# Performance work log

Measured on AMD Instinct MI355X. Metric: run time of the kernel, lower is better.

Reference implementation:

```python
import jax, jax.numpy as jnp
import numpy as np

B, S, D, F, T, NS, L, H = 8, 1024, 1024, 4096, 64, 512, 32, 16
TAG_RATE = 0.5      # config.tagging_rate
GSR = 0.5           # config.gate_scaling_rate
ATT_EPS = 1e-12     # config.layer_norm_eps (att_norm)
ENC_EPS = 1e-5      # torch TransformerEncoderLayer default


def _ln(x, g, b, eps):
    m = x.mean(-1, keepdims=True)
    v = x.var(-1, keepdims=True)
    return (x - m) * jax.lax.rsqrt(v + eps) * g + b


def _rope(x):
    # standard rotary embedding over the full hidden dim
    d = x.shape[-1]
    s = x.shape[1]
    inv = 1.0 / (10000.0 ** (jnp.arange(0, d, 2, dtype=jnp.float32) / d))
    ang = jnp.arange(s, dtype=jnp.float32)[:, None] * inv[None, :]  # [S, D/2]
    sin, cos = jnp.sin(ang), jnp.cos(ang)
    x1, x2 = x[..., 0::2], x[..., 1::2]
    return jnp.stack([x1 * cos - x2 * sin, x1 * sin + x2 * cos], axis=-1).reshape(x.shape)


def setup_inputs() -> dict:
    key = jax.random.key(0)
    ks = jax.random.split(key, 24)
    p = lambda k, shp: (0.02 * jax.random.normal(k, shp, dtype=jnp.float32))
    inp = {
        'word_embedding': jax.random.normal(ks[0], (B, S, D), dtype=jnp.float32),
        'attention_mask': jnp.ones((B, S), dtype=jnp.int32),
        'span_batch': jax.random.randint(ks[1], (NS,), 0, B, dtype=jnp.int32),
        'span_start': jax.random.randint(ks[2], (NS,), 0, S - L, dtype=jnp.int32),
        'span_tag': jax.random.randint(ks[3], (NS,), 0, T, dtype=jnp.int32),
        'tag_emb': p(ks[4], (T, D)),
        'gate_w': p(ks[5], (D, 1)),
        'gate_b': jnp.zeros((1,), jnp.float32),
        'attn_ln_g': jnp.ones((D,), jnp.float32),
        'attn_ln_b': jnp.zeros((D,), jnp.float32),
        'in_proj_w': p(ks[6], (3 * D, D)),
        'in_proj_b': jnp.zeros((3 * D,), jnp.float32),
        'out_proj_w': p(ks[7], (D, D)),
        'out_proj_b': jnp.zeros((D,), jnp.float32),
        'enc_ln1_g': jnp.ones((D,), jnp.float32),
        'enc_ln1_b': jnp.zeros((D,), jnp.float32),
        'lin1_w': p(ks[8], (F, D)),
        'lin1_b': jnp.zeros((F,), jnp.float32),
        'lin2_w': p(ks[9], (D, F)),
        'lin2_b': jnp.zeros((D,), jnp.float32),
        'enc_ln2_g': jnp.ones((D,), jnp.float32),
        'enc_ln2_b': jnp.zeros((D,), jnp.float32),
    }
    return inp


def _mha(x, pad, in_proj_w, in_proj_b, out_proj_w, out_proj_b):
    b, s, d = x.shape
    hd = d // H
    qkv = x @ in_proj_w.T + in_proj_b                       # [B,S,3D]
    q, k, v = jnp.split(qkv, 3, axis=-1)
    rs = lambda t: t.reshape(b, s, H, hd).transpose(0, 2, 1, 3)  # [B,H,S,hd]
    q, k, v = rs(q), rs(k), rs(v)
    scores = jnp.einsum('bhqd,bhkd->bhqk', q, k) / jnp.sqrt(jnp.float32(hd))
    scores = jnp.where(pad[:, None, None, :], jnp.float32(-1e30), scores)
    attn = jax.nn.softmax(scores, axis=-1)
    o = jnp.einsum('bhqk,bhkd->bhqd', attn, v).transpose(0, 2, 1, 3).reshape(b, s, d)
    return o @ out_proj_w.T + out_proj_b


def reference(word_embedding, attention_mask, span_batch, span_start, span_tag,
              tag_emb, gate_w, gate_b, attn_ln_g, attn_ln_b,
              in_proj_w, in_proj_b, out_proj_w, out_proj_b,
              enc_ln1_g, enc_ln1_b, lin1_w, lin1_b, lin2_w, lin2_b,
              enc_ln2_g, enc_ln2_b):
    raw = word_embedding                        # dropout off (eval)
    we = _rope(word_embedding)
    # ragged gather -> gate -> scatter-add over fixed-length spans
    tok = span_start[:, None] + jnp.arange(L, dtype=jnp.int32)[None, :]  # [NS,L]
    X = we[span_batch[:, None], tok]            # [NS,L,D]
    gate = GSR * jax.nn.sigmoid(X @ gate_w + gate_b) + (1.0 - GSR) / 2.0  # [NS,L,1]
    res = gate * tag_emb[span_tag][:, None, :] * jnp.float32(L)          # [NS,L,D]
    taged = jnp.zeros_like(word_embedding).at[span_batch[:, None], tok].add(res)
    out_emb = raw + taged * TAG_RATE            # if_merge_by_add
    out_emb = _ln(out_emb, attn_ln_g, attn_ln_b, ATT_EPS)
    pad = attention_mask == 0
    # torch TransformerEncoderLayer (post-norm, relu)
    a = _mha(out_emb, pad, in_proj_w, in_proj_b, out_proj_w, out_proj_b)
    x = _ln(out_emb + a, enc_ln1_g, enc_ln1_b, ENC_EPS)
    ff = jax.nn.relu(x @ lin1_w.T + lin1_b) @ lin2_w.T + lin2_b
    enc = _ln(x + ff, enc_ln2_g, enc_ln2_b, ENC_EPS)
    return enc + out_emb
```

## Files before the change

### kernel.cpp

```cpp
#include <hip/hip_runtime.h>

#define DEV __device__ __forceinline__

typedef short bf16x8 __attribute__((ext_vector_type(8)));
typedef float f32x4 __attribute__((ext_vector_type(4)));
typedef unsigned short u16;
typedef unsigned int u32;

typedef __attribute__((address_space(3))) void lds_void;
typedef __attribute__((address_space(1))) void gbl_void;

DEV void async_copy16(void* lds_dst, const void* g_src) {
    __builtin_amdgcn_global_load_lds((gbl_void*)g_src, (lds_void*)lds_dst, 16, 0, 0);
}

DEV u16 f2bf(float x) {
    u32 u = __float_as_uint(x);
    return (u16)((u + 0x7fffu + ((u >> 16) & 1u)) >> 16);
}
DEV u16 f2bf_fast(float x) {
    return (u16)((__float_as_uint(x) + 0x8000u) >> 16);
}
DEV float bf2f(u16 v) { return __uint_as_float(((u32)v) << 16); }

__global__ __launch_bounds__(256) void f2bf_kernel(const float* __restrict__ src,
                                                   u16* __restrict__ dst, int n4) {
    const int i = blockIdx.x * 256 + threadIdx.x;
    if (i < n4) {
        const float4 v = ((const float4*)src)[i];
        ushort4 o;
        o.x = f2bf(v.x); o.y = f2bf(v.y); o.z = f2bf(v.z); o.w = f2bf(v.w);
        ((ushort4*)dst)[i] = o;
    }
}

__global__ __launch_bounds__(256) void span_kernel(
    const float* __restrict__ we, const int* __restrict__ sb,
    const int* __restrict__ ss, const int* __restrict__ stg,
    const float* __restrict__ tag_emb, const float* __restrict__ gate_w,
    const float* __restrict__ gate_b, float* __restrict__ out_pre) {
    __shared__ float red[4];
    const int n = blockIdx.x >> 5;
    const int l = blockIdx.x & 31;
    const int t = threadIdx.x;
    const int b = sb[n];
    const int s = ss[n] + l;
    const int tag = stg[n];
    const long base = ((long)b * 1024 + s) * 1024;
    float dot = 0.f;
#pragma unroll
    for (int pp = 0; pp < 2; ++pp) {
        const int p = t + pp * 256;
        const float e1 = we[base + 2 * p];
        const float e2 = we[base + 2 * p + 1];
        const float inv = exp2f((float)p * (-13.287712379549449f / 512.0f));
        const float ang = (float)s * inv;
        const float sa = sinf(ang), ca = cosf(ang);
        const float r1 = e1 * ca - e2 * sa;
        const float r2 = e1 * sa + e2 * ca;
        dot += r1 * gate_w[2 * p] + r2 * gate_w[2 * p + 1];
    }
#pragma unroll
    for (int off = 32; off > 0; off >>= 1) dot += __shfl_xor(dot, off, 64);
    if ((t & 63) == 0) red[t >> 6] = dot;
    __syncthreads();
    const float z = red[0] + red[1] + red[2] + red[3] + gate_b[0];
    const float gate = 0.25f + 0.5f / (1.f + __expf(-z));
    const float coef = gate * 16.f;
    const float* te = tag_emb + (long)tag * 1024;
#pragma unroll
    for (int c = 0; c < 4; ++c) {
        const int d = t + c * 256;
        atomicAdd(&out_pre[base + d], coef * te[d]);
    }
}

template <bool WRITE_F32, bool WRITE_BF, bool FINAL>
__global__ __launch_bounds__(256) void ln_kernel(
    const float* __restrict__ X, const float* __restrict__ g,
    const float* __restrict__ bta, float eps, float* __restrict__ Yf,
    u16* __restrict__ Ybf, const u16* __restrict__ addend) {
    __shared__ float red[8];
    const long row = blockIdx.x;
    const int t = threadIdx.x;
    const float4 x = ((const float4*)(X + row * 1024))[t];
    float s = x.x + x.y + x.z + x.w;
#pragma unroll
    for (int off = 32; off > 0; off >>= 1) s += __shfl_xor(s, off, 64);
    if ((t & 63) == 0) red[t >> 6] = s;
    __syncthreads();
    const float mean = (red[0] + red[1] + red[2] + red[3]) * (1.f / 1024.f);
    float4 dx;
    dx.x = x.x - mean; dx.y = x.y - mean; dx.z = x.z - mean; dx.w = x.w - mean;
    float ss = dx.x * dx.x + dx.y * dx.y + dx.z * dx.z + dx.w * dx.w;
#pragma unroll
    for (int off = 32; off > 0; off >>= 1) ss += __shfl_xor(ss, off, 64);
    if ((t & 63) == 0) red[4 + (t >> 6)] = ss;
    __syncthreads();
    const float var = (red[4] + red[5] + red[6] + red[7]) * (1.f / 1024.f);
    const float rstd = rsqrtf(var + eps);
    const float4 gv = ((const float4*)g)[t];
    const float4 bv = ((const float4*)bta)[t];
    float4 y;
    y.x = dx.x * rstd * gv.x + bv.x;
    y.y = dx.y * rstd * gv.y + bv.y;
    y.z = dx.z * rstd * gv.z + bv.z;
    y.w = dx.w * rstd * gv.w + bv.w;
    if (FINAL) {
        const ushort4 a = ((const ushort4*)(addend + row * 1024))[t];
        y.x += bf2f(a.x); y.y += bf2f(a.y); y.z += bf2f(a.z); y.w += bf2f(a.w);
    }
    if (WRITE_F32) ((float4*)(Yf + row * 1024))[t] = y;
    if (WRITE_BF) {
        ushort4 o;
        o.x = f2bf(y.x); o.y = f2bf(y.y); o.z = f2bf(y.z); o.w = f2bf(y.w);
        ((ushort4*)(Ybf + row * 1024))[t] = o;
    }
}

template <bool OUT_BF16, bool RELU, bool HAS_RES>
__global__ __launch_bounds__(256, 2) void gemm_nt(
    const u16* __restrict__ A, const u16* __restrict__ B,
    const float* __restrict__ bias, const u16* __restrict__ res,
    void* __restrict__ Cout, int N, int K) {
    __shared__ u16 Al[8192];
    __shared__ u16 Bl[8192];
    const int tid = threadIdx.x;
    const int wave = tid >> 6;
    const int lane = tid & 63;
    const int quad = lane >> 4;
    const int lq = lane & 15;
    const int wm = wave >> 1;
    const int wn = wave & 1;
    const long rowBase = (long)blockIdx.x * 128;
    const long colBase = (long)blockIdx.y * 128;

    f32x4 acc[4][4];
    const f32x4 fzero = {0.f, 0.f, 0.f, 0.f};
#pragma unroll
    for (int i = 0; i < 4; ++i)
#pragma unroll
        for (int j = 0; j < 4; ++j) acc[i][j] = fzero;

    const int rX = tid >> 3;
    const int pX = (tid & 7) ^ (rX & 7);
    const u16* gA = A + (rowBase + rX) * (long)K + pX * 8;
    const u16* gB = B + (colBase + rX) * (long)K + pX * 8;
    u16* ldsA = Al + wave * 512;
    u16* ldsB = Bl + wave * 512;

    for (int kt = 0; kt < K; kt += 64) {
        __syncthreads();
#pragma unroll
        for (int c = 0; c < 4; ++c) {
            async_copy16(ldsA + c * 2048, gA + (long)c * 32 * K + kt);
            async_copy16(ldsB + c * 2048, gB + (long)c * 32 * K + kt);
        }
        __syncthreads();
#pragma unroll
        for (int ks = 0; ks < 2; ++ks) {
            bf16x8 af[4], bfr[4];
#pragma unroll
            for (int i = 0; i < 4; ++i) {
                const int r = wm * 64 + i * 16 + lq;
                af[i] = *(const bf16x8*)&Al[r * 64 + (((ks * 4 + quad) ^ (lq & 7)) * 8)];
            }
#pragma unroll
            for (int j = 0; j < 4; ++j) {
                const int r = wn * 64 + j * 16 + lq;
                bfr[j] = *(const bf16x8*)&Bl[r * 64 + (((ks * 4 + quad) ^ (lq & 7)) * 8)];
            }
#pragma unroll
            for (int i = 0; i < 4; ++i)
#pragma unroll
                for (int j = 0; j < 4; ++j)
                    acc[i][j] = __builtin_amdgcn_mfma_f32_16x16x32_bf16(
                        af[i], bfr[j], acc[i][j], 0, 0, 0);
        }
    }

    float biasv[4];
#pragma unroll
    for (int j = 0; j < 4; ++j) biasv[j] = bias[colBase + wn * 64 + j * 16 + lq];
#pragma unroll
    for (int i = 0; i < 4; ++i) {
        const long grow = rowBase + wm * 64 + i * 16 + quad * 4;
#pragma unroll
        for (int j = 0; j < 4; ++j) {
            const long gcol = colBase + wn * 64 + j * 16 + lq;
#pragma unroll
            for (int r = 0; r < 4; ++r) {
                float v = acc[i][j][r] + biasv[j];
                if (RELU) v = fmaxf(v, 0.f);
                if (HAS_RES) v += bf2f(res[(grow + r) * N + gcol]);
                if (OUT_BF16)
                    ((u16*)Cout)[(grow + r) * N + gcol] = f2bf(v);
                else
                    ((float*)Cout)[(grow + r) * N + gcol] = v;
            }
        }
    }
}

#define PH_SYNC()                                          \
    do {                                                   \
        __builtin_amdgcn_s_barrier();                      \
        asm volatile("s_waitcnt lgkmcnt(0)" ::: "memory"); \
        __builtin_amdgcn_sched_barrier(0);                 \
    } while (0)

template <bool RELU>
__global__ __launch_bounds__(512, 2) void gemm_nt8(
    const u16* __restrict__ A, const u16* __restrict__ B,
    const float* __restrict__ bias, u16* __restrict__ Cout, int N, int K) {
    __shared__ u16 Al[2][16384];
    __shared__ u16 Bl[2][16384];
    const int tid = threadIdx.x;
    const int wave = tid >> 6;
    const int lane = tid & 63;
    const int quad = lane >> 4;
    const int lq = lane & 15;
    const int lq7 = lq & 7;
    const int wm = wave >> 2;
    const int wn = wave & 3;
    const long rowBase = (long)blockIdx.x * 256;
    const long colBase = (long)blockIdx.y * 256;
    const int NT = K >> 6;

    const int rs = tid >> 3;
    const int js = (tid & 7) ^ (rs & 7);
    const u16* gA = A + (rowBase + rs) * (long)K + js * 8;
    const u16* gB = B + (colBase + rs) * (long)K + js * 8;

    f32x4 acc[8][4];
    const f32x4 fz = {0.f, 0.f, 0.f, 0.f};
#pragma unroll
    for (int i = 0; i < 8; ++i)
#pragma unroll
        for (int j = 0; j < 4; ++j) acc[i][j] = fz;

    auto stA = [&](int buf, int h, int t) {
        u16* d = &Al[buf][h * 8192 + wave * 512];
        const u16* s = gA + (long)h * 128 * K + t * 64;
        async_copy16(d, s);
        async_copy16(d + 4096, s + (long)64 * K);
    };
    auto stB = [&](int buf, int h, int t) {
        u16* d = &Bl[buf][h * 8192 + wave * 512];
        const u16* s = gB + (long)h * 128 * K + t * 64;
        async_copy16(d, s);
        async_copy16(d + 4096, s + (long)64 * K);
    };
    auto ldA = [&](int buf, int i, int kh) {
        const int r = wm * 128 + i * 16 + lq;
        return *(const bf16x8*)&Al[buf][r * 64 + ((((kh << 2) | quad) ^ lq7) << 3)];
    };
    auto ldB = [&](int buf, int j, int kh) {
        const int r = wn * 64 + j * 16 + lq;
        return *(const bf16x8*)&Bl[buf][r * 64 + ((((kh << 2) | quad) ^ lq7) << 3)];
    };

    stA(0, 0, 0); stA(0, 1, 0); stB(0, 0, 0); stB(0, 1, 0);
    stA(1, 0, 1);
    asm volatile("s_waitcnt vmcnt(2)" ::: "memory");
    __builtin_amdgcn_s_barrier();

    bf16x8 at[8], ab[8], bl[4], br[4];
    for (int it = 0; it < (NT >> 1); ++it) {
        const int t1 = 2 * it + 1;
        int t2 = 2 * it + 2; if (t2 >= NT) t2 -= NT;
        int t3 = 2 * it + 3; if (t3 >= NT) t3 -= NT;

#pragma unroll
        for (int i = 0; i < 4; ++i) { at[2 * i] = ldA(0, i, 0); at[2 * i + 1] = ldA(0, i, 1); }
#pragma unroll
        for (int j = 0; j < 2; ++j) { bl[2 * j] = ldB(0, j, 0); bl[2 * j + 1] = ldB(0, j, 1); }
        stA(1, 1, t1);
        PH_SYNC();
        __builtin_amdgcn_s_setprio(1);
#pragma unroll
        for (int i = 0; i < 4; ++i)
#pragma unroll
            for (int j = 0; j < 2; ++j)
#pragma unroll
                for (int kh = 0; kh < 2; ++kh)
                    acc[i][j] = __builtin_amdgcn_mfma_f32_16x16x32_bf16(
                        at[2 * i + kh], bl[2 * j + kh], acc[i][j], 0, 0, 0);
        __builtin_amdgcn_s_setprio(0);
        __builtin_amdgcn_s_barrier();
#pragma unroll
        for (int j = 0; j < 2; ++j) { br[2 * j] = ldB(0, j + 2, 0); br[2 * j + 1] = ldB(0, j + 2, 1); }
        stB(1, 0, t1);
        PH_SYNC();
        __builtin_amdgcn_s_setprio(1);
#pragma unroll
        for (int i = 0; i < 4; ++i)
#pragma unroll
            for (int j = 0; j < 2; ++j)
#pragma unroll
                for (int kh = 0; kh < 2; ++kh)
                    acc[i][j + 2] = __builtin_amdgcn_mfma_f32_16x16x32_bf16(
                        at[2 * i + kh], br[2 * j + kh], acc[i][j + 2], 0, 0, 0);
        __builtin_amdgcn_s_setprio(0);
        __builtin_amdgcn_s_barrier();
#pragma unroll
        for (int i = 0; i < 4; ++i) { ab[2 * i] = ldA(0, i + 4, 0); ab[2 * i + 1] = ldA(0, i + 4, 1); }
        stB(1, 1, t1);
        PH_SYNC();
        __builtin_amdgcn_s_setprio(1);
#pragma unroll
        for (int i = 0; i < 4; ++i)
#pragma unroll
            for (int j = 0; j < 2; ++j)
#pragma unroll
                for (int kh = 0; kh < 2; ++kh)
                    acc[i + 4][j] = __builtin_amdgcn_mfma_f32_16x16x32_bf16(
                        ab[2 * i + kh], bl[2 * j + kh], acc[i + 4][j], 0, 0, 0);
        __builtin_amdgcn_s_setprio(0);
        __builtin_amdgcn_s_barrier();
        stA(0, 0, t2);
        PH_SYNC();
        __builtin_amdgcn_s_setprio(1);
#pragma unroll
        for (int i = 0; i < 4; ++i)
#pragma unroll
            for (int j = 0; j < 2; ++j)
#pragma unroll
                for (int kh = 0; kh < 2; ++kh)
                    acc[i + 4][j + 2] = __builtin_amdgcn_mfma_f32_16x16x32_bf16(
                        ab[2 * i + kh], br[2 * j + kh], acc[i + 4][j + 2], 0, 0, 0);
        __builtin_amdgcn_s_setprio(0);
        asm volatile("s_waitcnt vmcnt(2)" ::: "memory");
        __builtin_amdgcn_s_barrier();

#pragma unroll
        for (int i = 0; i < 4; ++i) { at[2 * i] = ldA(1, i, 0); at[2 * i + 1] = ldA(1, i, 1); }
#pragma unroll
        for (int j = 0; j < 2; ++j) { bl[2 * j] = ldB(1, j, 0); bl[2 * j + 1] = ldB(1, j, 1); }
        stA(0, 1, t2);
        PH_SYNC();
        __builtin_amdgcn_s_setprio(1);
#pragma unroll
        for (int i = 0; i < 4; ++i)
#pragma unroll
            for (int j = 0; j < 2; ++j)
#pragma unroll
                for (int kh = 0; kh < 2; ++kh)
                    acc[i][j] = __builtin_amdgcn_mfma_f32_16x16x32_bf16(
                        at[2 * i + kh], bl[2 * j + kh], acc[i][j], 0, 0, 0);
        __builtin_amdgcn_s_setprio(0);
        __builtin_amdgcn_s_barrier();
#pragma unroll
        for (int j = 0; j < 2; ++j) { br[2 * j] = ldB(1, j + 2, 0); br[2 * j + 1] = ldB(1, j + 2, 1); }
        stB(0, 0, t2);
        PH_SYNC();
        __builtin_amdgcn_s_setprio(1);
#pragma unroll
        for (int i = 0; i < 4; ++i)
#pragma unroll
            for (int j = 0; j < 2; ++j)
#pragma unroll
                for (int kh = 0; kh < 2; ++kh)
                    acc[i][j + 2] = __builtin_amdgcn_mfma_f32_16x16x32_bf16(
                        at[2 * i + kh], br[2 * j + kh], acc[i][j + 2], 0, 0, 0);
        __builtin_amdgcn_s_setprio(0);
        __builtin_amdgcn_s_barrier();
#pragma unroll
        for (int i = 0; i < 4; ++i) { ab[2 * i] = ldA(1, i + 4, 0); ab[2 * i + 1] = ldA(1, i + 4, 1); }
        stB(0, 1, t2);
        PH_SYNC();
        __builtin_amdgcn_s_setprio(1);
#pragma unroll
        for (int i = 0; i < 4; ++i)
#pragma unroll
            for (int j = 0; j < 2; ++j)
#pragma unroll
                for (int kh = 0; kh < 2; ++kh)
                    acc[i + 4][j] = __builtin_amdgcn_mfma_f32_16x16x32_bf16(
                        ab[2 * i + kh], bl[2 * j + kh], acc[i + 4][j], 0, 0, 0);
        __builtin_amdgcn_s_setprio(0);
        __builtin_amdgcn_s_barrier();
        stA(1, 0, t3);
        PH_SYNC();
        __builtin_amdgcn_s_setprio(1);
#pragma unroll
        for (int i = 0; i < 4; ++i)
#pragma unroll
            for (int j = 0; j < 2; ++j)
#pragma unroll
                for (int kh = 0; kh < 2; ++kh)
                    acc[i + 4][j + 2] = __builtin_amdgcn_mfma_f32_16x16x32_bf16(
                        ab[2 * i + kh], br[2 * j + kh], acc[i + 4][j + 2], 0, 0, 0);
        __builtin_amdgcn_s_setprio(0);
        asm volatile("s_waitcnt vmcnt(2)" ::: "memory");
        __builtin_amdgcn_s_barrier();
    }

    asm volatile("s_waitcnt vmcnt(0)" ::: "memory");
    float bv[4];
#pragma unroll
    for (int j = 0; j < 4; ++j) bv[j] = bias[colBase + wn * 64 + j * 16 + lq];
#pragma unroll
    for (int i = 0; i < 8; ++i) {
        const long grow = rowBase + wm * 128 + i * 16 + quad * 4;
#pragma unroll
        for (int j = 0; j < 4; ++j) {
            const long gcol = colBase + wn * 64 + j * 16 + lq;
#pragma unroll
            for (int r = 0; r < 4; ++r) {
                float v = acc[i][j][r] + bv[j];
                if (RELU) v = fmaxf(v, 0.f);
                Cout[(grow + r) * N + gcol] = f2bf(v);
            }
        }
    }
}

__global__ __launch_bounds__(256) void vtrans_kernel(const u16* __restrict__ QKV,
                                                     u16* __restrict__ Vt) {
    __shared__ u16 tile[64][72];
    const int bid = blockIdx.x;
    const int st = bid & 15;
    const int h = (bid >> 4) & 15;
    const int b = bid >> 8;
    const int t = threadIdx.x;
    const int sl = t >> 2;
    const int dc = (t & 3) * 16;
    const u16* src = QKV + ((long)(b * 1024 + st * 64 + sl)) * 3072 + 2048 + h * 64 + dc;
    *(uint4*)&tile[sl][dc] = *(const uint4*)src;
    *(uint4*)&tile[sl][dc + 8] = *(const uint4*)(src + 8);
    __syncthreads();
    const int dl = t >> 2;
    const int sc = (t & 3) * 16;
    union { u16 u[16]; uint4 q[2]; } tmp;
#pragma unroll
    for (int i = 0; i < 16; ++i) tmp.u[i] = tile[sc + i][dl];
    u16* dst = Vt + ((long)(b * 16 + h) * 64 + dl) * 1024 + st * 64 + sc;
    *(uint4*)dst = tmp.q[0];
    *(uint4*)(dst + 8) = tmp.q[1];
}

__global__ __launch_bounds__(256, 4) void attn_kernel(
    const u16* __restrict__ QKV, const u16* __restrict__ Vt,
    const int* __restrict__ mask, u16* __restrict__ Out) {
    __shared__ u16 KL[4096];
    __shared__ u16 VL[4096];
    __shared__ u16 PL[4][16 * 72];
    const int tid = threadIdx.x;
    const int wid = tid >> 6;
    const int lane = tid & 63;
    const int quad = lane >> 4;
    const int lq = lane & 15;
    const int slot0 = quad ^ (lq & 7);
    const int slot1 = slot0 ^ 4;

    const int bid = blockIdx.x;
    const int qb = bid & 7;
    const int h = (bid >> 3) & 15;
    const int b = bid >> 7;
    const int qbase = qb * 128 + wid * 32;

    bf16x8 aq[2][2];
#pragma unroll
    for (int t = 0; t < 2; ++t) {
        const u16* qp = QKV + ((long)(b * 1024 + qbase + t * 16 + lq)) * 3072 +
                        h * 64 + quad * 8;
        aq[t][0] = *(const bf16x8*)qp;
        aq[t][1] = *(const bf16x8*)(qp + 32);
    }

    const int c0 = tid, c1 = 256 + tid;
    const int r0 = c0 >> 3, j0 = (c0 & 7) ^ (r0 & 7);
    const int r1 = c1 >> 3, j1 = (c1 & 7) ^ (r1 & 7);
    const u16* srcK0 = QKV + ((long)(b * 1024 + r0)) * 3072 + 1024 + h * 64 + j0 * 8;
    const u16* srcK1 = QKV + ((long)(b * 1024 + r1)) * 3072 + 1024 + h * 64 + j1 * 8;
    const u16* srcV0 = Vt + ((long)(b * 16 + h) * 64 + r0) * 1024 + j0 * 8;
    const u16* srcV1 = Vt + ((long)(b * 16 + h) * 64 + r1) * 1024 + j1 * 8;
    u16* ldsK0 = KL + wid * 512;
    u16* ldsK1 = KL + 2048 + wid * 512;
    u16* ldsV0 = VL + wid * 512;
    u16* ldsV1 = VL + 2048 + wid * 512;

    const f32x4 fzero = {0.f, 0.f, 0.f, 0.f};
    f32x4 acc[2][4];
#pragma unroll
    for (int t = 0; t < 2; ++t)
#pragma unroll
        for (int j = 0; j < 4; ++j) acc[t][j] = fzero;
    float lsum[2][4] = {{0.f, 0.f, 0.f, 0.f}, {0.f, 0.f, 0.f, 0.f}};
    u16* myP = PL[wid];
    const int* mrow = mask + b * 1024;

    for (int kt = 0; kt < 1024; kt += 64) {
        __syncthreads();
        async_copy16(ldsK0, srcK0 + (long)kt * 3072);
        async_copy16(ldsK1, srcK1 + (long)kt * 3072);
        async_copy16(ldsV0, srcV0 + kt);
        async_copy16(ldsV1, srcV1 + kt);
        __syncthreads();

        bf16x8 kf0[4], kf1[4];
#pragma unroll
        for (int ct = 0; ct < 4; ++ct) {
            const int rowb = (ct * 16 + lq) * 64;
            kf0[ct] = *(const bf16x8*)&KL[rowb + slot0 * 8];
            kf1[ct] = *(const bf16x8*)&KL[rowb + slot1 * 8];
        }
        float mw[4];
#pragma unroll
        for (int ct = 0; ct < 4; ++ct) mw[ct] = mrow[kt + ct * 16 + lq] ? 1.f : 0.f;

#pragma unroll
        for (int t = 0; t < 2; ++t) {
            f32x4 s[4];
#pragma unroll
            for (int ct = 0; ct < 4; ++ct) {
                s[ct] = __builtin_amdgcn_mfma_f32_16x16x32_bf16(aq[t][0], kf0[ct],
                                                                fzero, 0, 0, 0);
                s[ct] = __builtin_amdgcn_mfma_f32_16x16x32_bf16(aq[t][1], kf1[ct],
                                                                s[ct], 0, 0, 0);
            }
            asm volatile("s_waitcnt lgkmcnt(0)" ::: "memory");
#pragma unroll
            for (int ct = 0; ct < 4; ++ct)
#pragma unroll
                for (int r = 0; r < 4; ++r) {
                    const float p = mw[ct] * __expf(s[ct][r] * 0.125f);
                    lsum[t][r] += p;
                    myP[(quad * 4 + r) * 72 + ct * 16 + lq] = f2bf_fast(p);
                }
            asm volatile("s_waitcnt lgkmcnt(0)" ::: "memory");
            const bf16x8 pf0 = *(const bf16x8*)&myP[lq * 72 + quad * 8];
            const bf16x8 pf1 = *(const bf16x8*)&myP[lq * 72 + 32 + quad * 8];
#pragma unroll
            for (int j = 0; j < 4; ++j) {
                const int rowb = (j * 16 + lq) * 64;
                const bf16x8 vf0 = *(const bf16x8*)&VL[rowb + slot0 * 8];
                const bf16x8 vf1 = *(const bf16x8*)&VL[rowb + slot1 * 8];
                acc[t][j] = __builtin_amdgcn_mfma_f32_16x16x32_bf16(pf0, vf0,
                                                                    acc[t][j], 0, 0, 0);
                acc[t][j] = __builtin_amdgcn_mfma_f32_16x16x32_bf16(pf1, vf1,
                                                                    acc[t][j], 0, 0, 0);
            }
        }
    }

#pragma unroll
    for (int t = 0; t < 2; ++t) {
        float inv[4];
#pragma unroll
        for (int r = 0; r < 4; ++r) {
            float l = lsum[t][r];
#pragma unroll
            for (int off = 1; off < 16; off <<= 1) l += __shfl_xor(l, off, 16);
            inv[r] = 1.f / l;
        }
        const long orow = (long)b * 1024 + qbase + t * 16 + quad * 4;
#pragma unroll
        for (int j = 0; j < 4; ++j)
#pragma unroll
            for (int r = 0; r < 4; ++r)
                Out[(orow + r) * 1024 + h * 64 + j * 16 + lq] =
                    f2bf_fast(acc[t][j][r] * inv[r]);
    }
}

extern "C" void kernel_launch(void* const* d_in, const int* in_sizes, int n_in,
                              void* d_out, int out_size, void* d_ws, size_t ws_size,
                              hipStream_t stream) {
    const float* we        = (const float*)d_in[0];
    const int*   amask     = (const int*)d_in[1];
    const int*   span_b    = (const int*)d_in[2];
    const int*   span_s    = (const int*)d_in[3];
    const int*   span_t    = (const int*)d_in[4];
    const float* tag_emb   = (const float*)d_in[5];
    const float* gate_w    = (const float*)d_in[6];
    const float* gate_b    = (const float*)d_in[7];
    const float* attn_ln_g = (const float*)d_in[8];
    const float* attn_ln_b = (const float*)d_in[9];
    const float* in_proj_w = (const float*)d_in[10];
    const float* in_proj_b = (const float*)d_in[11];
    const float* out_proj_w= (const float*)d_in[12];
    const float* out_proj_b= (const float*)d_in[13];
    const float* enc1_g    = (const float*)d_in[14];
    const float* enc1_b    = (const float*)d_in[15];
    const float* lin1_w    = (const float*)d_in[16];
    const float* lin1_b    = (const float*)d_in[17];
    const float* lin2_w    = (const float*)d_in[18];
    const float* lin2_b    = (const float*)d_in[19];
    const float* enc2_g    = (const float*)d_in[20];
    const float* enc2_b    = (const float*)d_in[21];
    float* out = (float*)d_out;

    char* ws = (char*)d_ws;
    size_t off = 0;
    auto alloc = [&](size_t bytes) {
        void* p = ws + off;
        off += (bytes + 255) & ~(size_t)255;
        return p;
    };
    const size_t MT = 8192;
    u16* oe_bf   = (u16*)alloc(MT * 1024 * 2);
    u16* ax_bf   = (u16*)alloc(MT * 1024 * 2);
    char* region = (char*)alloc((size_t)67108864);
    u16* qkv_bf  = (u16*)region;
    u16* vt_bf   = (u16*)(region + (size_t)MT * 3072 * 2);
    u16* ff1_bf  = (u16*)region;
    u16* wb_inproj  = (u16*)alloc((size_t)3072 * 1024 * 2);
    u16* wb_outproj = (u16*)alloc((size_t)1024 * 1024 * 2);
    u16* wb_lin1    = (u16*)alloc((size_t)4096 * 1024 * 2);
    u16* wb_lin2    = (u16*)alloc((size_t)1024 * 4096 * 2);

    hipMemcpyAsync(out, we, MT * 1024 * 4, hipMemcpyDeviceToDevice, stream);
    f2bf_kernel<<<3072, 256, 0, stream>>>(in_proj_w, wb_inproj, 3072 * 1024 / 4);
    f2bf_kernel<<<1024, 256, 0, stream>>>(out_proj_w, wb_outproj, 1024 * 1024 / 4);
    f2bf_kernel<<<4096, 256, 0, stream>>>(lin1_w, wb_lin1, 4096 * 1024 / 4);
    f2bf_kernel<<<4096, 256, 0, stream>>>(lin2_w, wb_lin2, 1024 * 4096 / 4);
    span_kernel<<<16384, 256, 0, stream>>>(we, span_b, span_s, span_t, tag_emb,
                                           gate_w, gate_b, out);
    ln_kernel<false, true, false><<<8192, 256, 0, stream>>>(
        out, attn_ln_g, attn_ln_b, 1e-12f, nullptr, oe_bf, nullptr);
    dim3 g1(32, 12);
    gemm_nt8<false><<<g1, 512, 0, stream>>>(oe_bf, wb_inproj, in_proj_b,
                                            qkv_bf, 3072, 1024);
    vtrans_kernel<<<2048, 256, 0, stream>>>(qkv_bf, vt_bf);
    attn_kernel<<<1024, 256, 0, stream>>>(qkv_bf, vt_bf, amask, ax_bf);
    dim3 g2(64, 8);
    gemm_nt<false, false, true><<<g2, 256, 0, stream>>>(ax_bf, wb_outproj, out_proj_b,
                                                        oe_bf, out, 1024, 1024);
    ln_kernel<false, true, false><<<8192, 256, 0, stream>>>(
        out, enc1_g, enc1_b, 1e-5f, nullptr, ax_bf, nullptr);
    dim3 g3(32, 16);
    gemm_nt8<true><<<g3, 512, 0, stream>>>(ax_bf, wb_lin1, lin1_b,
                                           ff1_bf, 4096, 1024);
    gemm_nt<false, false, true><<<g2, 256, 0, stream>>>(ff1_bf, wb_lin2, lin2_b,
                                                        ax_bf, out, 1024, 4096);
    ln_kernel<true, false, true><<<8192, 256, 0, stream>>>(
        out, enc2_g, enc2_b, 1e-5f, out, nullptr, oe_bf);
}
```

Before: 570.1 us.

## Fuse span tagging, LN and weight casts; fold V transpose into QKV GEMM

Replaces the memcpy, four weight-cast kernels, the atomic span scatter and the first layernorm with a single prep kernel. In it each token row finds its overlapping spans via ballots and adds the tag embeddings in registers before normalising. The QKV GEMM epilogue writes V directly in transposed layout, which removes the separate vtrans kernel. The 8-wave GEMM's async-load schedule is reordered so B for the next tile is prefetched first. Attention block indexing is permuted to group heads and batches per query block. These changes cut launches, atomics and global traffic, at the cost of strided scattered stores for V and a per-row scan over all 512 spans.

```diff
diff --git a/kernel.cpp b/kernel.cpp
--- a/kernel.cpp
+++ b/kernel.cpp
@@ -6,6 +6,7 @@
 typedef float f32x4 __attribute__((ext_vector_type(4)));
 typedef unsigned short u16;
 typedef unsigned int u32;
+typedef unsigned long long u64;
 
 typedef __attribute__((address_space(3))) void lds_void;
 typedef __attribute__((address_space(1))) void gbl_void;
@@ -23,42 +24,62 @@
 }
 DEV float bf2f(u16 v) { return __uint_as_float(((u32)v) << 16); }
 
-__global__ __launch_bounds__(256) void f2bf_kernel(const float* __restrict__ src,
-                                                   u16* __restrict__ dst, int n4) {
-    const int i = blockIdx.x * 256 + threadIdx.x;
-    if (i < n4) {
+__global__ __launch_bounds__(256) void prep_kernel(
+    const float* __restrict__ we, const int* __restrict__ sb,
+    const int* __restrict__ ss, const int* __restrict__ stg,
+    const float* __restrict__ tag_emb, const float* __restrict__ gate_w,
+    const float* __restrict__ gate_b, const float* __restrict__ g,
+    const float* __restrict__ bta,
+    const float* __restrict__ w0, const float* __restrict__ w1,
+    const float* __restrict__ w2, const float* __restrict__ w3,
+    u16* __restrict__ oe_bf, u16* __restrict__ o0, u16* __restrict__ o1,
+    u16* __restrict__ o2, u16* __restrict__ o3) {
+    const int blk = blockIdx.x;
+    const int t = threadIdx.x;
+
+    if (blk >= 8192) {
+        int base = blk - 8192;
+        const float* src; u16* dst;
+        if (base < 3072)      { src = w0; dst = o0; }
+        else if (base < 4096) { src = w1; dst = o1; base -= 3072; }
+        else if (base < 8192) { src = w2; dst = o2; base -= 4096; }
+        else                  { src = w3; dst = o3; base -= 8192; }
+        const int i = base * 256 + t;
         const float4 v = ((const float4*)src)[i];
         ushort4 o;
         o.x = f2bf(v.x); o.y = f2bf(v.y); o.z = f2bf(v.z); o.w = f2bf(v.w);
         ((ushort4*)dst)[i] = o;
-    }
-}
-
-__global__ __launch_bounds__(256) void span_kernel(
-    const float* __restrict__ we, const int* __restrict__ sb,
-    const int* __restrict__ ss, const int* __restrict__ stg,
-    const float* __restrict__ tag_emb, const float* __restrict__ gate_w,
-    const float* __restrict__ gate_b, float* __restrict__ out_pre) {
-    __shared__ float red[4];
-    const int n = blockIdx.x >> 5;
-    const int l = blockIdx.x & 31;
-    const int t = threadIdx.x;
-    const int b = sb[n];
-    const int s = ss[n] + l;
-    const int tag = stg[n];
-    const long base = ((long)b * 1024 + s) * 1024;
-    float dot = 0.f;
-#pragma unroll
-    for (int pp = 0; pp < 2; ++pp) {
-        const int p = t + pp * 256;
-        const float e1 = we[base + 2 * p];
-        const float e2 = we[base + 2 * p + 1];
-        const float inv = exp2f((float)p * (-13.287712379549449f / 512.0f));
-        const float ang = (float)s * inv;
-        const float sa = sinf(ang), ca = cosf(ang);
-        const float r1 = e1 * ca - e2 * sa;
-        const float r2 = e1 * sa + e2 * ca;
-        dot += r1 * gate_w[2 * p] + r2 * gate_w[2 * p + 1];
+        return;
+    }
+
+    __shared__ float red[8];
+    __shared__ u64 smask[8];
+    const int row = blk;
+    const int b = row >> 10;
+    const int s = row & 1023;
+
+    {
+        const bool m0 = (sb[t] == b) && ((u32)(s - ss[t]) < 32u);
+        const bool m1 = (sb[t + 256] == b) && ((u32)(s - ss[t + 256]) < 32u);
+        const u64 b0 = __ballot(m0);
+        const u64 b1 = __ballot(m1);
+        if ((t & 63) == 0) { smask[t >> 6] = b0; smask[4 + (t >> 6)] = b1; }
+    }
+
+    float4 x = ((const float4*)(we + (long)row * 1024))[t];
+    const float4 gw = ((const float4*)gate_w)[t];
+    float dot;
+    {
+        const float p0 = (float)(2 * t);
+        const float p1 = (float)(2 * t + 1);
+        const float inv0 = exp2f(p0 * (-13.287712379549449f / 512.0f));
+        const float inv1 = exp2f(p1 * (-13.287712379549449f / 512.0f));
+        const float a0 = (float)s * inv0, a1 = (float)s * inv1;
+        const float s0 = sinf(a0), c0 = cosf(a0);
+        const float s1 = sinf(a1), c1 = cosf(a1);
+        const float r1a = x.x * c0 - x.y * s0, r2a = x.x * s0 + x.y * c0;
+        const float r1b = x.z * c1 - x.w * s1, r2b = x.z * s1 + x.w * c1;
+        dot = r1a * gw.x + r2a * gw.y + r1b * gw.z + r2b * gw.w;
     }
 #pragma unroll
     for (int off = 32; off > 0; off >>= 1) dot += __shfl_xor(dot, off, 64);
@@ -67,12 +88,47 @@
     const float z = red[0] + red[1] + red[2] + red[3] + gate_b[0];
     const float gate = 0.25f + 0.5f / (1.f + __expf(-z));
     const float coef = gate * 16.f;
-    const float* te = tag_emb + (long)tag * 1024;
-#pragma unroll
-    for (int c = 0; c < 4; ++c) {
-        const int d = t + c * 256;
-        atomicAdd(&out_pre[base + d], coef * te[d]);
-    }
+
+    float4 add = {0.f, 0.f, 0.f, 0.f};
+#pragma unroll
+    for (int gi = 0; gi < 8; ++gi) {
+        u64 m = smask[gi];
+        const int nb = (gi & 3) * 64 + (gi >> 2) * 256;
+        while (m) {
+            const int bit = __ffsll(m) - 1;
+            m &= m - 1;
+            const int tag = stg[nb + bit];
+            const float4 te = ((const float4*)(tag_emb + (long)tag * 1024))[t];
+            add.x += te.x; add.y += te.y; add.z += te.z; add.w += te.w;
+        }
+    }
+    x.x += coef * add.x; x.y += coef * add.y;
+    x.z += coef * add.z; x.w += coef * add.w;
+
+    __syncthreads();
+    float sm = x.x + x.y + x.z + x.w;
+#pragma unroll
+    for (int off = 32; off > 0; off >>= 1) sm += __shfl_xor(sm, off, 64);
+    if ((t & 63) == 0) red[t >> 6] = sm;
+    __syncthreads();
+    const float mean = (red[0] + red[1] + red[2] + red[3]) * (1.f / 1024.f);
+    float4 dx;
+    dx.x = x.x - mean; dx.y = x.y - mean; dx.z = x.z - mean; dx.w = x.w - mean;
+    float ss2 = dx.x * dx.x + dx.y * dx.y + dx.z * dx.z + dx.w * dx.w;
+#pragma unroll
+    for (int off = 32; off > 0; off >>= 1) ss2 += __shfl_xor(ss2, off, 64);
+    if ((t & 63) == 0) red[4 + (t >> 6)] = ss2;
+    __syncthreads();
+    const float var = (red[4] + red[5] + red[6] + red[7]) * (1.f / 1024.f);
+    const float rstd = rsqrtf(var + 1e-12f);
+    const float4 gv = ((const float4*)g)[t];
+    const float4 bv = ((const float4*)bta)[t];
+    ushort4 o;
+    o.x = f2bf(dx.x * rstd * gv.x + bv.x);
+    o.y = f2bf(dx.y * rstd * gv.y + bv.y);
+    o.z = f2bf(dx.z * rstd * gv.z + bv.z);
+    o.w = f2bf(dx.w * rstd * gv.w + bv.w);
+    ((ushort4*)(oe_bf + (long)row * 1024))[t] = o;
 }
 
 template <bool WRITE_F32, bool WRITE_BF, bool FINAL>
@@ -118,11 +174,11 @@
     }
 }
 
-template <bool OUT_BF16, bool RELU, bool HAS_RES>
+template <bool OUT_BF16, bool RELU, bool HAS_RES, bool VTRANS>
 __global__ __launch_bounds__(256, 2) void gemm_nt(
     const u16* __restrict__ A, const u16* __restrict__ B,
     const float* __restrict__ bias, const u16* __restrict__ res,
-    void* __restrict__ Cout, int N, int K) {
+    void* __restrict__ Cout, int N, int K, u16* __restrict__ vt) {
     __shared__ u16 Al[8192];
     __shared__ u16 Bl[8192];
     const int tid = threadIdx.x;
@@ -193,26 +249,28 @@
                 float v = acc[i][j][r] + biasv[j];
                 if (RELU) v = fmaxf(v, 0.f);
                 if (HAS_RES) v += bf2f(res[(grow + r) * N + gcol]);
-                if (OUT_BF16)
+                if (VTRANS && gcol >= 2048) {
+                    const int hh = (int)(gcol - 2048) >> 6;
+                    const int dd = (int)(gcol - 2048) & 63;
+                    const long rr = grow + r;
+                    const int bb = (int)(rr >> 10);
+                    const int sR = (int)(rr & 1023);
+                    vt[(((long)bb * 16 + hh) * 64 + dd) * 1024 + sR] = f2bf(v);
+                } else if (OUT_BF16) {
                     ((u16*)Cout)[(grow + r) * N + gcol] = f2bf(v);
-                else
+                } else {
                     ((float*)Cout)[(grow + r) * N + gcol] = v;
+                }
             }
         }
     }
 }
 
-#define PH_SYNC()                                          \
-    do {                                                   \
-        __builtin_amdgcn_s_barrier();                      \
-        asm volatile("s_waitcnt lgkmcnt(0)" ::: "memory"); \
-        __builtin_amdgcn_sched_barrier(0);                 \
-    } while (0)
-
-template <bool RELU>
+template <bool RELU, bool VTRANS>
 __global__ __launch_bounds__(512, 2) void gemm_nt8(
     const u16* __restrict__ A, const u16* __restrict__ B,
-    const float* __restrict__ bias, u16* __restrict__ Cout, int N, int K) {
+    const float* __restrict__ bias, u16* __restrict__ Cout, int N, int K,
+    u16* __restrict__ vt) {
     __shared__ u16 Al[2][16384];
     __shared__ u16 Bl[2][16384];
     const int tid = threadIdx.x;
@@ -241,13 +299,13 @@
 
     auto stA = [&](int buf, int h, int t) {
         u16* d = &Al[buf][h * 8192 + wave * 512];
-        const u16* s = gA + (long)h * 128 * K + t * 64;
+        const u16* s = gA + (long)h * 128 * K + (long)t * 64;
         async_copy16(d, s);
         async_copy16(d + 4096, s + (long)64 * K);
     };
     auto stB = [&](int buf, int h, int t) {
         u16* d = &Bl[buf][h * 8192 + wave * 512];
-        const u16* s = gB + (long)h * 128 * K + t * 64;
+        const u16* s = gB + (long)h * 128 * K + (long)t * 64;
         async_copy16(d, s);
         async_copy16(d + 4096, s + (long)64 * K);
     };
@@ -260,9 +318,16 @@
         return *(const bf16x8*)&Bl[buf][r * 64 + ((((kh << 2) | quad) ^ lq7) << 3)];
     };
 
+#define PH_SYNC()                               \
+    do {                                        \
+        __builtin_amdgcn_s_barrier();           \
+        asm volatile("s_waitcnt lgkmcnt(0)");   \
+    } while (0)
+
     stA(0, 0, 0); stA(0, 1, 0); stB(0, 0, 0); stB(0, 1, 0);
-    stA(1, 0, 1);
-    asm volatile("s_waitcnt vmcnt(2)" ::: "memory");
+    stB(1, 0, 1); stB(1, 1, 1);
+    asm volatile("s_waitcnt vmcnt(4)");
+    __builtin_amdgcn_sched_barrier(0);
     __builtin_amdgcn_s_barrier();
 
     bf16x8 at[8], ab[8], bl[4], br[4];
@@ -275,7 +340,7 @@
         for (int i = 0; i < 4; ++i) { at[2 * i] = ldA(0, i, 0); at[2 * i + 1] = ldA(0, i, 1); }
 #pragma unroll
         for (int j = 0; j < 2; ++j) { bl[2 * j] = ldB(0, j, 0); bl[2 * j + 1] = ldB(0, j, 1); }
-        stA(1, 1, t1);
+        stA(1, 0, t1);
         PH_SYNC();
         __builtin_amdgcn_s_setprio(1);
 #pragma unroll
@@ -290,7 +355,7 @@
         __builtin_amdgcn_s_barrier();
 #pragma unroll
         for (int j = 0; j < 2; ++j) { br[2 * j] = ldB(0, j + 2, 0); br[2 * j + 1] = ldB(0, j + 2, 1); }
-        stB(1, 0, t1);
+        stA(1, 1, t1);
         PH_SYNC();
         __builtin_amdgcn_s_setprio(1);
 #pragma unroll
@@ -305,7 +370,7 @@
         __builtin_amdgcn_s_barrier();
 #pragma unroll
         for (int i = 0; i < 4; ++i) { ab[2 * i] = ldA(0, i + 4, 0); ab[2 * i + 1] = ldA(0, i + 4, 1); }
-        stB(1, 1, t1);
+        stB(0, 0, t2);
         PH_SYNC();
         __builtin_amdgcn_s_setprio(1);
 #pragma unroll
@@ -318,7 +383,7 @@
                         ab[2 * i + kh], bl[2 * j + kh], acc[i + 4][j], 0, 0, 0);
         __builtin_amdgcn_s_setprio(0);
         __builtin_amdgcn_s_barrier();
-        stA(0, 0, t2);
+        stB(0, 1, t2);
         PH_SYNC();
         __builtin_amdgcn_s_setprio(1);
 #pragma unroll
@@ -330,14 +395,15 @@
                     acc[i + 4][j + 2] = __builtin_amdgcn_mfma_f32_16x16x32_bf16(
                         ab[2 * i + kh], br[2 * j + kh], acc[i + 4][j + 2], 0, 0, 0);
         __builtin_amdgcn_s_setprio(0);
-        asm volatile("s_waitcnt vmcnt(2)" ::: "memory");
+        asm volatile("s_waitcnt vmcnt(4)");
+        __builtin_amdgcn_sched_barrier(0);
         __builtin_amdgcn_s_barrier();
 
 #pragma unroll
         for (int i = 0; i < 4; ++i) { at[2 * i] = ldA(1, i, 0); at[2 * i + 1] = ldA(1, i, 1); }
 #pragma unroll
         for (int j = 0; j < 2; ++j) { bl[2 * j] = ldB(1, j, 0); bl[2 * j + 1] = ldB(1, j, 1); }
-        stA(0, 1, t2);
+        stA(0, 0, t2);
         PH_SYNC();
         __builtin_amdgcn_s_setprio(1);
 #pragma unroll
@@ -352,7 +418,7 @@
         __builtin_amdgcn_s_barrier();
 #pragma unroll
         for (int j = 0; j < 2; ++j) { br[2 * j] = ldB(1, j + 2, 0); br[2 * j + 1] = ldB(1, j + 2, 1); }
-        stB(0, 0, t2);
+        stA(0, 1, t2);
         PH_SYNC();
         __builtin_amdgcn_s_setprio(1);
 #pragma unroll
@@ -367,7 +433,7 @@
         __builtin_amdgcn_s_barrier();
 #pragma unroll
         for (int i = 0; i < 4; ++i) { ab[2 * i] = ldA(1, i + 4, 0); ab[2 * i + 1] = ldA(1, i + 4, 1); }
-        stB(0, 1, t2);
+        stB(1, 0, t3);
         PH_SYNC();
         __builtin_amdgcn_s_setprio(1);
 #pragma unroll
@@ -380,7 +446,7 @@
                         ab[2 * i + kh], bl[2 * j + kh], acc[i + 4][j], 0, 0, 0);
         __builtin_amdgcn_s_setprio(0);
         __builtin_amdgcn_s_barrier();
-        stA(1, 0, t3);
+        stB(1, 1, t3);
         PH_SYNC();
         __builtin_amdgcn_s_setprio(1);
 #pragma unroll
@@ -392,11 +458,13 @@
                     acc[i + 4][j + 2] = __builtin_amdgcn_mfma_f32_16x16x32_bf16(
                         ab[2 * i + kh], br[2 * j + kh], acc[i + 4][j + 2], 0, 0, 0);
         __builtin_amdgcn_s_setprio(0);
-        asm volatile("s_waitcnt vmcnt(2)" ::: "memory");
-        __builtin_amdgcn_s_barrier();
-    }
-
-    asm volatile("s_waitcnt vmcnt(0)" ::: "memory");
+        asm volatile("s_waitcnt vmcnt(4)");
+        __builtin_amdgcn_sched_barrier(0);
+        __builtin_amdgcn_s_barrier();
+    }
+#undef PH_SYNC
+
+    asm volatile("s_waitcnt vmcnt(0)");
     float bv[4];
 #pragma unroll
     for (int j = 0; j < 4; ++j) bv[j] = bias[colBase + wn * 64 + j * 16 + lq];
@@ -410,34 +478,19 @@
             for (int r = 0; r < 4; ++r) {
                 float v = acc[i][j][r] + bv[j];
                 if (RELU) v = fmaxf(v, 0.f);
-                Cout[(grow + r) * N + gcol] = f2bf(v);
+                if (VTRANS && gcol >= 2048) {
+                    const int hh = (int)(gcol - 2048) >> 6;
+                    const int dd = (int)(gcol - 2048) & 63;
+                    const long rr = grow + r;
+                    const int bb = (int)(rr >> 10);
+                    const int sR = (int)(rr & 1023);
+                    vt[(((long)bb * 16 + hh) * 64 + dd) * 1024 + sR] = f2bf(v);
+                } else {
+                    Cout[(grow + r) * N + gcol] = f2bf(v);
+                }
             }
         }
     }
-}
-
-__global__ __launch_bounds__(256) void vtrans_kernel(const u16* __restrict__ QKV,
-                                                     u16* __restrict__ Vt) {
-    __shared__ u16 tile[64][72];
-    const int bid = blockIdx.x;
-    const int st = bid & 15;
-    const int h = (bid >> 4) & 15;
-    const int b = bid >> 8;
-    const int t = threadIdx.x;
-    const int sl = t >> 2;
-    const int dc = (t & 3) * 16;
-    const u16* src = QKV + ((long)(b * 1024 + st * 64 + sl)) * 3072 + 2048 + h * 64 + dc;
-    *(uint4*)&tile[sl][dc] = *(const uint4*)src;
-    *(uint4*)&tile[sl][dc + 8] = *(const uint4*)(src + 8);
-    __syncthreads();
-    const int dl = t >> 2;
-    const int sc = (t & 3) * 16;
-    union { u16 u[16]; uint4 q[2]; } tmp;
-#pragma unroll
-    for (int i = 0; i < 16; ++i) tmp.u[i] = tile[sc + i][dl];
-    u16* dst = Vt + ((long)(b * 16 + h) * 64 + dl) * 1024 + st * 64 + sc;
-    *(uint4*)dst = tmp.q[0];
-    *(uint4*)(dst + 8) = tmp.q[1];
 }
 
 __global__ __launch_bounds__(256, 4) void attn_kernel(
@@ -455,9 +508,9 @@
     const int slot1 = slot0 ^ 4;
 
     const int bid = blockIdx.x;
-    const int qb = bid & 7;
-    const int h = (bid >> 3) & 15;
-    const int b = bid >> 7;
+    const int qb = bid >> 7;
+    const int h = bid & 15;
+    const int b = (bid >> 4) & 7;
     const int qbase = qb * 128 + wid * 32;
 
     bf16x8 aq[2][2];
@@ -611,30 +664,24 @@
     u16* wb_lin1    = (u16*)alloc((size_t)4096 * 1024 * 2);
     u16* wb_lin2    = (u16*)alloc((size_t)1024 * 4096 * 2);
 
-    hipMemcpyAsync(out, we, MT * 1024 * 4, hipMemcpyDeviceToDevice, stream);
-    f2bf_kernel<<<3072, 256, 0, stream>>>(in_proj_w, wb_inproj, 3072 * 1024 / 4);
-    f2bf_kernel<<<1024, 256, 0, stream>>>(out_proj_w, wb_outproj, 1024 * 1024 / 4);
-    f2bf_kernel<<<4096, 256, 0, stream>>>(lin1_w, wb_lin1, 4096 * 1024 / 4);
-    f2bf_kernel<<<4096, 256, 0, stream>>>(lin2_w, wb_lin2, 1024 * 4096 / 4);
-    span_kernel<<<16384, 256, 0, stream>>>(we, span_b, span_s, span_t, tag_emb,
-                                           gate_w, gate_b, out);
-    ln_kernel<false, true, false><<<8192, 256, 0, stream>>>(
-        out, attn_ln_g, attn_ln_b, 1e-12f, nullptr, oe_bf, nullptr);
+    prep_kernel<<<20480, 256, 0, stream>>>(
+        we, span_b, span_s, span_t, tag_emb, gate_w, gate_b,
+        attn_ln_g, attn_ln_b, in_proj_w, out_proj_w, lin1_w, lin2_w,
+        oe_bf, wb_inproj, wb_outproj, wb_lin1, wb_lin2);
     dim3 g1(32, 12);
-    gemm_nt8<false><<<g1, 512, 0, stream>>>(oe_bf, wb_inproj, in_proj_b,
-                                            qkv_bf, 3072, 1024);
-    vtrans_kernel<<<2048, 256, 0, stream>>>(qkv_bf, vt_bf);
+    gemm_nt8<false, true><<<g1, 512, 0, stream>>>(
+        oe_bf, wb_inproj, in_proj_b, qkv_bf, 3072, 1024, vt_bf);
     attn_kernel<<<1024, 256, 0, stream>>>(qkv_bf, vt_bf, amask, ax_bf);
     dim3 g2(64, 8);
-    gemm_nt<false, false, true><<<g2, 256, 0, stream>>>(ax_bf, wb_outproj, out_proj_b,
-                                                        oe_bf, out, 1024, 1024);
+    gemm_nt<false, false, true, false><<<g2, 256, 0, stream>>>(
+        ax_bf, wb_outproj, out_proj_b, oe_bf, out, 1024, 1024, nullptr);
     ln_kernel<false, true, false><<<8192, 256, 0, stream>>>(
         out, enc1_g, enc1_b, 1e-5f, nullptr, ax_bf, nullptr);
     dim3 g3(32, 16);
-    gemm_nt8<true><<<g3, 512, 0, stream>>>(ax_bf, wb_lin1, lin1_b,
-                                           ff1_bf, 4096, 1024);
-    gemm_nt<false, false, true><<<g2, 256, 0, stream>>>(ff1_bf, wb_lin2, lin2_b,
-                                                        ax_bf, out, 1024, 4096);
+    gemm_nt8<true, false><<<g3, 512, 0, stream>>>(
+        ax_bf, wb_lin1, lin1_b, ff1_bf, 4096, 1024, nullptr);
+    gemm_nt<false, false, true, false><<<g2, 256, 0, stream>>>(
+        ff1_bf, wb_lin2, lin2_b, ax_bf, out, 1024, 4096, nullptr);
     ln_kernel<true, false, true><<<8192, 256, 0, stream>>>(
         out, enc2_g, enc2_b, 1e-5f, out, nullptr, oe_bf);
 }
```

Measured after the change: 522.0 us. -8.4%, faster.
